# Performance work log

Measured on AMD Instinct MI355X. Metric: run time of the kernel, lower is better.

## Reference

```python
import jax, jax.numpy as jnp
import numpy as np

N = 100000      # nodes
E = 1600000     # edges (avg degree 16)
D_IN = 128
D_H = 128
D_OUT = 64


def setup_inputs() -> dict:
    key = jax.random.key(0)
    ks = jax.random.split(key, 8)
    x = jax.random.normal(ks[0], (N, D_IN), dtype=jnp.float32)
    edge_index = jax.random.randint(ks[1], (2, E), 0, N, dtype=jnp.int64)
    # PyG GraphConv params: lin_rel (with bias) applied to aggregated messages,
    # lin_root (no bias) applied to self features. Kaiming-ish init scale.
    s1 = 1.0 / np.sqrt(D_IN)
    s2 = 1.0 / np.sqrt(D_H)
    W_rel1 = jax.random.uniform(ks[2], (D_H, D_IN), jnp.float32, -s1, s1)
    b_rel1 = jax.random.uniform(ks[3], (D_H,), jnp.float32, -s1, s1)
    W_root1 = jax.random.uniform(ks[4], (D_H, D_IN), jnp.float32, -s1, s1)
    W_rel2 = jax.random.uniform(ks[5], (D_OUT, D_H), jnp.float32, -s2, s2)
    b_rel2 = jax.random.uniform(ks[6], (D_OUT,), jnp.float32, -s2, s2)
    W_root2 = jax.random.uniform(ks[7], (D_OUT, D_H), jnp.float32, -s2, s2)
    return {
        "x": x, "edge_index": edge_index,
        "W_rel1": W_rel1, "b_rel1": b_rel1, "W_root1": W_root1,
        "W_rel2": W_rel2, "b_rel2": b_rel2, "W_root2": W_root2,
    }


def _graph_conv(x, src, dst, W_rel, b_rel, W_root):
    # sum-aggregate neighbor features x[src] into destination nodes,
    # then out = lin_rel(agg) + lin_root(x)  (PyG GraphConv, aggr='add')
    agg = jax.ops.segment_sum(x[src], dst, num_segments=x.shape[0])  # [N, d_in]
    return agg @ W_rel.T + b_rel + x @ W_root.T                      # [N, d_out]


def reference(x, edge_index, W_rel1, b_rel1, W_root1, W_rel2, b_rel2, W_root2):
    src, dst = edge_index[0], edge_index[1]
    h = jax.nn.relu(_graph_conv(x, src, dst, W_rel1, b_rel1, W_root1))  # [N, D_H]
    out = _graph_conv(h, src, dst, W_rel2, b_rel2, W_root2)             # [N, D_OUT]
    # reshape(-1, 1, output_dim) + cat over relations (relations == 1)
    return out.reshape(-1, 1, D_OUT)
```

## Files before the change

### kernel.cpp

```cpp
#include <hip/hip_runtime.h>
#include <hip/hip_bf16.h>


#define BM 128
#define BK 32
#define NPASS 8
#define FILL_GRID 2048

typedef unsigned short ushort_t;

__device__ __forceinline__ ushort_t f2bf(float f) {
    unsigned int u = __float_as_uint(f);
    unsigned int r = (u + 0x7fff + ((u >> 16) & 1)) >> 16;
    return (ushort_t)r;
}

__device__ __forceinline__ float bf2f(ushort_t v) {
    return __uint_as_float(((unsigned int)v) << 16);
}

__device__ __forceinline__ void bf2x(unsigned int v, float& lo, float& hi) {
    lo = __uint_as_float(v << 16);
    hi = __uint_as_float(v & 0xffff0000u);
}


__global__ __launch_bounds__(256) void hist_kernel(const int* __restrict__ dst,
                                                   int* __restrict__ deg, int E, int N) {
    const int pass = blockIdx.x & (NPASS - 1);
    const int chunk = blockIdx.x >> 3;
    const int rangeSize = (N + NPASS - 1) / NPASS;
    const int lo = pass * rangeSize;
    const int hi = (lo + rangeSize < N) ? lo + rangeSize : N;
    const int base = chunk * 1024 + threadIdx.x * 4;
    if (base + 3 < E) {
        const int4 d4 = *(const int4*)(dst + base);
        if (d4.x >= lo && d4.x < hi) atomicAdd(&deg[d4.x], 1);
        if (d4.y >= lo && d4.y < hi) atomicAdd(&deg[d4.y], 1);
        if (d4.z >= lo && d4.z < hi) atomicAdd(&deg[d4.z], 1);
        if (d4.w >= lo && d4.w < hi) atomicAdd(&deg[d4.w], 1);
    } else {
        for (int i = 0; i < 4; ++i) {
            int e = base + i;
            if (e < E) {
                int d = dst[e];
                if (d >= lo && d < hi) atomicAdd(&deg[d], 1);
            }
        }
    }
}

__global__ __launch_bounds__(256) void scan1_kernel(const int* __restrict__ deg,
                                                    int* __restrict__ bsum, int N) {
    int t = threadIdx.x;
    int base = blockIdx.x * 1024 + t * 4;
    int s = 0;
    if (base + 3 < N) {
        int4 v = *(const int4*)(deg + base);
        s = v.x + v.y + v.z + v.w;
    } else {
#pragma unroll
        for (int i = 0; i < 4; ++i)
            if (base + i < N) s += deg[base + i];
    }
#pragma unroll
    for (int d = 32; d > 0; d >>= 1) s += __shfl_down(s, d);
    __shared__ int wsum[4];
    int lane = t & 63, w = t >> 6;
    if (lane == 0) wsum[w] = s;
    __syncthreads();
    if (t == 0) bsum[blockIdx.x] = wsum[0] + wsum[1] + wsum[2] + wsum[3];
}

__global__ __launch_bounds__(256) void scan2_kernel(const int* __restrict__ bsum,
                                                    int* __restrict__ boff,
                                                    int* __restrict__ offN, int B) {
    __shared__ int s[256];
    int t = threadIdx.x;
    int v = (t < B) ? bsum[t] : 0;
    s[t] = v;
    __syncthreads();
    for (int d = 1; d < 256; d <<= 1) {
        int u = (t >= d) ? s[t - d] : 0;
        __syncthreads();
        s[t] += u;
        __syncthreads();
    }
    if (t < B) boff[t] = s[t] - v;
    if (t == B - 1) *offN = s[t];
}

__global__ __launch_bounds__(256) void scan3_kernel(const int* __restrict__ deg,
                                                    const int* __restrict__ boff,
                                                    int* __restrict__ off,
                                                    int* __restrict__ cursor, int N) {
    int t = threadIdx.x;
    int base = blockIdx.x * 1024 + t * 4;
    int d0 = 0, d1 = 0, d2 = 0, d3 = 0;
    if (base + 3 < N) {
        int4 v = *(const int4*)(deg + base);
        d0 = v.x; d1 = v.y; d2 = v.z; d3 = v.w;
    } else {
        if (base + 0 < N) d0 = deg[base + 0];
        if (base + 1 < N) d1 = deg[base + 1];
        if (base + 2 < N) d2 = deg[base + 2];
    }
    int s = d0 + d1 + d2 + d3;
    int lane = t & 63, w = t >> 6;
    int incl = s;
#pragma unroll
    for (int d = 1; d < 64; d <<= 1) {
        int u = __shfl_up(incl, d);
        if (lane >= d) incl += u;
    }
    __shared__ int wsum[4];
    if (lane == 63) wsum[w] = incl;
    __syncthreads();
    int wpre = 0;
#pragma unroll
    for (int i = 0; i < 3; ++i)
        if (i < w) wpre += wsum[i];
    int excl = incl - s + wpre + boff[blockIdx.x];
    int e0 = excl, e1 = e0 + d0, e2 = e1 + d1, e3 = e2 + d2;
    if (base + 3 < N) {
        *(int4*)(off + base) = make_int4(e0, e1, e2, e3);
        *(int4*)(cursor + base) = make_int4(e0, e1, e2, e3);
    } else {
        if (base + 0 < N) { off[base + 0] = e0; cursor[base + 0] = e0; }
        if (base + 1 < N) { off[base + 1] = e1; cursor[base + 1] = e1; }
        if (base + 2 < N) { off[base + 2] = e2; cursor[base + 2] = e2; }
    }
}

__global__ __launch_bounds__(256) void fill_kernel(const int* __restrict__ src,
                                                   const int* __restrict__ dst,
                                                   int* __restrict__ cursor,
                                                   int* __restrict__ csr, int E, int N) {
    const int pass = blockIdx.x & (NPASS - 1);
    const int rangeSize = (N + NPASS - 1) / NPASS;
    const int lo = pass * rangeSize;
    const int hi = (lo + rangeSize < N) ? lo + rangeSize : N;
    const int nChunk = (E + 1023) >> 10;
    for (int chunk = blockIdx.x >> 3; chunk < nChunk; chunk += FILL_GRID / NPASS) {
        const int base = chunk * 1024 + threadIdx.x * 4;
        if (base + 3 < E) {
            const int4 s4 = *(const int4*)(src + base);
            const int4 d4 = *(const int4*)(dst + base);
            if (d4.x >= lo && d4.x < hi) csr[atomicAdd(&cursor[d4.x], 1)] = s4.x;
            if (d4.y >= lo && d4.y < hi) csr[atomicAdd(&cursor[d4.y], 1)] = s4.y;
            if (d4.z >= lo && d4.z < hi) csr[atomicAdd(&cursor[d4.z], 1)] = s4.z;
            if (d4.w >= lo && d4.w < hi) csr[atomicAdd(&cursor[d4.w], 1)] = s4.w;
        } else {
            for (int i = 0; i < 4; ++i) {
                int e = base + i;
                if (e < E) {
                    int d = dst[e];
                    if (d >= lo && d < hi) csr[atomicAdd(&cursor[d], 1)] = src[e];
                }
            }
        }
    }
}


template <int BN, int EPI, int OB, int AB>
__global__ __launch_bounds__(256, 2)
void gemm_k(const float* __restrict__ X, const float* __restrict__ W,
            const void* __restrict__ AGGv, const float* __restrict__ bias,
            void* __restrict__ OUTv, int Nrows) {
    __shared__ float xs[BK][BM + 4];
    __shared__ float wsh[BK][BN + 4];

    const int tid = threadIdx.x;
    const int tc = tid & 15;
    const int tr = tid >> 4;
    const int rowBase = blockIdx.x * BM;
    constexpr int CG = BN / 64;

    float acc[8][4 * CG];
#pragma unroll
    for (int i = 0; i < 8; ++i)
#pragma unroll
        for (int j = 0; j < 4 * CG; ++j) acc[i][j] = 0.f;

    const int srow = tid >> 3;
    const int skq = (tid & 7) * 4;

    for (int kc = 0; kc < 128; kc += BK) {
#pragma unroll
        for (int i = 0; i < 4; ++i) {
            int r = srow + i * 32;
            int g = rowBase + r;
            g = g < Nrows ? g : Nrows - 1;
            const float4 v = *(const float4*)(X + (size_t)g * 128 + kc + skq);
            xs[skq + 0][r] = v.x;
            xs[skq + 1][r] = v.y;
            xs[skq + 2][r] = v.z;
            xs[skq + 3][r] = v.w;
        }
#pragma unroll
        for (int i = 0; i < BN / 32; ++i) {
            int j = srow + i * 32;
            const float4 v = *(const float4*)(W + (size_t)j * 128 + kc + skq);
            wsh[skq + 0][j] = v.x;
            wsh[skq + 1][j] = v.y;
            wsh[skq + 2][j] = v.z;
            wsh[skq + 3][j] = v.w;
        }
        __syncthreads();
#pragma unroll
        for (int k = 0; k < BK; ++k) {
            const float4 xa = *(const float4*)&xs[k][tr * 8];
            const float4 xb = *(const float4*)&xs[k][tr * 8 + 4];
            float xr[8] = {xa.x, xa.y, xa.z, xa.w, xb.x, xb.y, xb.z, xb.w};
            float wv[4 * CG];
            const float4 wa = *(const float4*)&wsh[k][tc * 4];
            wv[0] = wa.x; wv[1] = wa.y; wv[2] = wa.z; wv[3] = wa.w;
            if (CG == 2) {
                const float4 wb = *(const float4*)&wsh[k][64 + tc * 4];
                wv[4] = wb.x; wv[5] = wb.y; wv[6] = wb.z; wv[7] = wb.w;
            }
#pragma unroll
            for (int i = 0; i < 8; ++i)
#pragma unroll
                for (int j = 0; j < 4 * CG; ++j) acc[i][j] += xr[i] * wv[j];
        }
        __syncthreads();
    }

#pragma unroll
    for (int i = 0; i < 8; ++i) {
        int g = rowBase + tr * 8 + i;
        if (g >= Nrows) continue;
#pragma unroll
        for (int cg = 0; cg < CG; ++cg) {
            int c = cg * 64 + tc * 4;
            float4 r;
            r.x = acc[i][cg * 4 + 0];
            r.y = acc[i][cg * 4 + 1];
            r.z = acc[i][cg * 4 + 2];
            r.w = acc[i][cg * 4 + 3];
            if (EPI != 0) {
                float ax, ay, az, aw;
                if (AB) {
                    const ushort_t* A = (const ushort_t*)AGGv;
                    ushort4 a4 = *(const ushort4*)(A + (size_t)g * BN + c);
                    ax = bf2f(a4.x); ay = bf2f(a4.y); az = bf2f(a4.z); aw = bf2f(a4.w);
                } else {
                    const float4 a = *(const float4*)((const float*)AGGv + (size_t)g * BN + c);
                    ax = a.x; ay = a.y; az = a.z; aw = a.w;
                }
                const float4 bb = *(const float4*)(bias + c);
                r.x += ax + bb.x;
                r.y += ay + bb.y;
                r.z += az + bb.z;
                r.w += aw + bb.w;
                if (EPI == 1) {
                    r.x = r.x > 0.f ? r.x : 0.f;
                    r.y = r.y > 0.f ? r.y : 0.f;
                    r.z = r.z > 0.f ? r.z : 0.f;
                    r.w = r.w > 0.f ? r.w : 0.f;
                }
            }
            if (OB) {
                ushort_t* OUT = (ushort_t*)OUTv;
                ushort4 o;
                o.x = f2bf(r.x); o.y = f2bf(r.y); o.z = f2bf(r.z); o.w = f2bf(r.w);
                *(ushort4*)(OUT + (size_t)g * BN + c) = o;
            } else {
                float* OUT = (float*)OUTv;
                *(float4*)(OUT + (size_t)g * BN + c) = r;
            }
        }
    }
}


template <int D, int OB>
__global__ __launch_bounds__(256)
void agg_k(const ushort_t* __restrict__ F, const int* __restrict__ csr,
           const int* __restrict__ off, void* __restrict__ OUTv, int N) {
    constexpr int LPN = (D == 128) ? 32 : 16;
    constexpr int NPB = 256 / LPN;
    int n = blockIdx.x * NPB + (threadIdx.x / LPN);
    if (n >= N) return;
    int lane = threadIdx.x & (LPN - 1);
    int b = off[n], e = off[n + 1];
    const size_t col = (size_t)lane * 4;
    float a0 = 0.f, a1 = 0.f, a2 = 0.f, a3 = 0.f;
    int i = b;
    for (; i + 4 <= e; i += 4) {
        int s0 = csr[i], s1 = csr[i + 1], s2 = csr[i + 2], s3 = csr[i + 3];
        uint2 v0 = *(const uint2*)(F + (size_t)s0 * D + col);
        uint2 v1 = *(const uint2*)(F + (size_t)s1 * D + col);
        uint2 v2 = *(const uint2*)(F + (size_t)s2 * D + col);
        uint2 v3 = *(const uint2*)(F + (size_t)s3 * D + col);
        float l, h;
        bf2x(v0.x, l, h); a0 += l; a1 += h;
        bf2x(v0.y, l, h); a2 += l; a3 += h;
        bf2x(v1.x, l, h); a0 += l; a1 += h;
        bf2x(v1.y, l, h); a2 += l; a3 += h;
        bf2x(v2.x, l, h); a0 += l; a1 += h;
        bf2x(v2.y, l, h); a2 += l; a3 += h;
        bf2x(v3.x, l, h); a0 += l; a1 += h;
        bf2x(v3.y, l, h); a2 += l; a3 += h;
    }
    for (; i < e; ++i) {
        uint2 v = *(const uint2*)(F + (size_t)csr[i] * D + col);
        float l, h;
        bf2x(v.x, l, h); a0 += l; a1 += h;
        bf2x(v.y, l, h); a2 += l; a3 += h;
    }
    if (OB) {
        ushort_t* OUT = (ushort_t*)OUTv;
        ushort4 o;
        o.x = f2bf(a0); o.y = f2bf(a1); o.z = f2bf(a2); o.w = f2bf(a3);
        *(ushort4*)(OUT + (size_t)n * D + col) = o;
    } else {
        float* OUT = (float*)OUTv;
        float4 r; r.x = a0; r.y = a1; r.z = a2; r.w = a3;
        *(float4*)(OUT + (size_t)n * D + col) = r;
    }
}

extern "C" void kernel_launch(void* const* d_in, const int* in_sizes, int n_in,
                              void* d_out, int out_size, void* d_ws, size_t ws_size,
                              hipStream_t stream) {
    const float* x   = (const float*)d_in[0];
    const int*   ei  = (const int*)d_in[1];
    const float* Wr1 = (const float*)d_in[2];
    const float* br1 = (const float*)d_in[3];
    const float* Wo1 = (const float*)d_in[4];
    const float* Wr2 = (const float*)d_in[5];
    const float* br2 = (const float*)d_in[6];
    const float* Wo2 = (const float*)d_in[7];
    float* out = (float*)d_out;

    const int N = in_sizes[0] / 128;
    const int E = in_sizes[1] / 2;

    const int* srcv = ei;
    const int* dstv = ei + E;

    float*    h    = (float*)d_ws;
    ushort_t* qb   = (ushort_t*)(h + (size_t)N * 128);
    ushort_t* a1b  = qb + (size_t)N * 128;
    ushort_t* a2b  = a1b + (size_t)N * 128;
    int*      deg  = (int*)(a2b + (size_t)N * 64);
    int*      off  = deg + N;
    int*      cur  = off + N + 8;
    int*      csr  = cur + N;
    int*      bsum = csr + E;
    int*      boff = bsum + 256;

    const int gemmBlocks = (N + BM - 1) / BM;
    const int agg128Blocks = (N + 7) / 8;
    const int agg64Blocks = (N + 15) / 16;
    const int B = (N + 1023) / 1024;
    const int edgePassBlocks = ((E + 1023) / 1024) * NPASS;

    hipMemsetAsync(deg, 0, (size_t)N * sizeof(int), stream);
    hist_kernel<<<edgePassBlocks, 256, 0, stream>>>(dstv, deg, E, N);
    scan1_kernel<<<B, 256, 0, stream>>>(deg, bsum, N);
    scan2_kernel<<<1, 256, 0, stream>>>(bsum, boff, off + N, B);
    scan3_kernel<<<B, 256, 0, stream>>>(deg, boff, off, cur, N);
    fill_kernel<<<FILL_GRID, 256, 0, stream>>>(srcv, dstv, cur, csr, E, N);

    gemm_k<128, 0, 1, 0><<<gemmBlocks, 256, 0, stream>>>(x, Wr1, nullptr, nullptr, qb, N);
    agg_k<128, 1><<<agg128Blocks, 256, 0, stream>>>(qb, csr, off, a1b, N);
    gemm_k<128, 1, 0, 1><<<gemmBlocks, 256, 0, stream>>>(x, Wo1, a1b, br1, h, N);

    gemm_k<64, 0, 1, 0><<<gemmBlocks, 256, 0, stream>>>(h, Wr2, nullptr, nullptr, qb , N);
    agg_k<64, 1><<<agg64Blocks, 256, 0, stream>>>(qb , csr, off, a2b, N);
    gemm_k<64, 2, 0, 1><<<gemmBlocks, 256, 0, stream>>>(h, Wo2, a2b, br2, out, N);
}
```

Measured before the change: 502.5 us.

## Replace FP32 SIMT GEMMs with concatenated-weight bf16 MFMA GEMMs and separate epilogues

Converts x and weights to bf16 and concatenates the rel and root weight matrices so one MFMA GEMM per layer computes both projections. The bias, aggregation add and ReLU move into standalone elementwise epilogue kernels, and edge-index reads use nontemporal loads. This removes the scalar FP32 FMA GEMM cost and halves GEMM launches, but adds conversion and epilogue passes over memory. The root path now runs in bf16, which lowers precision.

```diff
diff --git a/kernel.cpp b/kernel.cpp
--- a/kernel.cpp
+++ b/kernel.cpp
@@ -2,12 +2,12 @@
 #include <hip/hip_bf16.h>
 
 
-#define BM 128
-#define BK 32
 #define NPASS 8
 #define FILL_GRID 2048
 
 typedef unsigned short ushort_t;
+using bfrag = __attribute__((ext_vector_type(8))) short;
+using f32x4 = __attribute__((ext_vector_type(4))) float;
 
 __device__ __forceinline__ ushort_t f2bf(float f) {
     unsigned int u = __float_as_uint(f);
@@ -22,6 +22,17 @@
 __device__ __forceinline__ void bf2x(unsigned int v, float& lo, float& hi) {
     lo = __uint_as_float(v << 16);
     hi = __uint_as_float(v & 0xffff0000u);
+}
+
+__device__ __forceinline__ int4 ldnt_int4(const int* p) {
+    unsigned long long a = __builtin_nontemporal_load((const unsigned long long*)p);
+    unsigned long long b = __builtin_nontemporal_load(((const unsigned long long*)p) + 1);
+    int4 r;
+    r.x = (int)(unsigned int)(a & 0xffffffffull);
+    r.y = (int)(unsigned int)(a >> 32);
+    r.z = (int)(unsigned int)(b & 0xffffffffull);
+    r.w = (int)(unsigned int)(b >> 32);
+    return r;
 }
 
 
@@ -34,7 +45,7 @@
     const int hi = (lo + rangeSize < N) ? lo + rangeSize : N;
     const int base = chunk * 1024 + threadIdx.x * 4;
     if (base + 3 < E) {
-        const int4 d4 = *(const int4*)(dst + base);
+        const int4 d4 = ldnt_int4(dst + base);
         if (d4.x >= lo && d4.x < hi) atomicAdd(&deg[d4.x], 1);
         if (d4.y >= lo && d4.y < hi) atomicAdd(&deg[d4.y], 1);
         if (d4.z >= lo && d4.z < hi) atomicAdd(&deg[d4.z], 1);
@@ -144,8 +155,8 @@
     for (int chunk = blockIdx.x >> 3; chunk < nChunk; chunk += FILL_GRID / NPASS) {
         const int base = chunk * 1024 + threadIdx.x * 4;
         if (base + 3 < E) {
-            const int4 s4 = *(const int4*)(src + base);
-            const int4 d4 = *(const int4*)(dst + base);
+            const int4 s4 = ldnt_int4(src + base);
+            const int4 d4 = ldnt_int4(dst + base);
             if (d4.x >= lo && d4.x < hi) csr[atomicAdd(&cursor[d4.x], 1)] = s4.x;
             if (d4.y >= lo && d4.y < hi) csr[atomicAdd(&cursor[d4.y], 1)] = s4.y;
             if (d4.z >= lo && d4.z < hi) csr[atomicAdd(&cursor[d4.z], 1)] = s4.z;
@@ -163,113 +174,78 @@
 }
 
 
-template <int BN, int EPI, int OB, int AB>
+__global__ __launch_bounds__(256) void cvt_kernel(const float* __restrict__ in,
+                                                  ushort_t* __restrict__ out, int n) {
+    int base = (blockIdx.x * 256 + threadIdx.x) * 4;
+    if (base + 3 < n) {
+        float4 v = *(const float4*)(in + base);
+        ushort4 o;
+        o.x = f2bf(v.x); o.y = f2bf(v.y); o.z = f2bf(v.z); o.w = f2bf(v.w);
+        *(ushort4*)(out + base) = o;
+    } else {
+        for (int i = 0; i < 4 && base + i < n; ++i) out[base + i] = f2bf(in[base + i]);
+    }
+}
+
+__global__ __launch_bounds__(256) void cvt_w_kernel(const float* __restrict__ Wr1,
+                                                    const float* __restrict__ Wo1,
+                                                    const float* __restrict__ Wr2,
+                                                    const float* __restrict__ Wo2,
+                                                    ushort_t* __restrict__ wcat1,
+                                                    ushort_t* __restrict__ wcat2) {
+    int i = blockIdx.x * 256 + threadIdx.x;
+    if (i < 16384) wcat1[i] = f2bf(Wr1[i]);
+    else if (i < 32768) wcat1[i] = f2bf(Wo1[i - 16384]);
+    else if (i < 40960) wcat2[i - 32768] = f2bf(Wr2[i - 32768]);
+    else if (i < 49152) wcat2[i - 32768] = f2bf(Wo2[i - 40960]);
+}
+
+
+template <int BN, int SPLIT, int O2F>
 __global__ __launch_bounds__(256, 2)
-void gemm_k(const float* __restrict__ X, const float* __restrict__ W,
-            const void* __restrict__ AGGv, const float* __restrict__ bias,
-            void* __restrict__ OUTv, int Nrows) {
-    __shared__ float xs[BK][BM + 4];
-    __shared__ float wsh[BK][BN + 4];
-
-    const int tid = threadIdx.x;
-    const int tc = tid & 15;
-    const int tr = tid >> 4;
-    const int rowBase = blockIdx.x * BM;
-    constexpr int CG = BN / 64;
-
-    float acc[8][4 * CG];
-#pragma unroll
-    for (int i = 0; i < 8; ++i)
-#pragma unroll
-        for (int j = 0; j < 4 * CG; ++j) acc[i][j] = 0.f;
-
-    const int srow = tid >> 3;
-    const int skq = (tid & 7) * 4;
-
-    for (int kc = 0; kc < 128; kc += BK) {
-#pragma unroll
-        for (int i = 0; i < 4; ++i) {
-            int r = srow + i * 32;
-            int g = rowBase + r;
-            g = g < Nrows ? g : Nrows - 1;
-            const float4 v = *(const float4*)(X + (size_t)g * 128 + kc + skq);
-            xs[skq + 0][r] = v.x;
-            xs[skq + 1][r] = v.y;
-            xs[skq + 2][r] = v.z;
-            xs[skq + 3][r] = v.w;
+void mfma_gemm(const ushort_t* __restrict__ A, const ushort_t* __restrict__ Wc,
+               ushort_t* __restrict__ O1, void* __restrict__ O2v, int Nrows) {
+    constexpr int NT = BN / 16;
+    const int w = threadIdx.x >> 6;
+    const int lane = threadIdx.x & 63;
+    const int m0 = blockIdx.x * 64 + w * 16;
+    const int lm = lane & 15;
+    const int lk8 = (lane >> 4) * 8;
+
+    f32x4 acc[NT];
+#pragma unroll
+    for (int t = 0; t < NT; ++t) {
+        acc[t][0] = 0.f; acc[t][1] = 0.f; acc[t][2] = 0.f; acc[t][3] = 0.f;
+    }
+
+    int ar = m0 + lm;
+    ar = ar < Nrows ? ar : Nrows - 1;
+    const ushort_t* Arow = A + (size_t)ar * 128;
+
+#pragma unroll
+    for (int kk = 0; kk < 4; ++kk) {
+        const bfrag af = *(const bfrag*)(Arow + kk * 32 + lk8);
+#pragma unroll
+        for (int t = 0; t < NT; ++t) {
+            const bfrag bf = *(const bfrag*)(Wc + ((size_t)(t * 16 + lm) << 7) + kk * 32 + lk8);
+            acc[t] = __builtin_amdgcn_mfma_f32_16x16x32_bf16(af, bf, acc[t], 0, 0, 0);
         }
-#pragma unroll
-        for (int i = 0; i < BN / 32; ++i) {
-            int j = srow + i * 32;
-            const float4 v = *(const float4*)(W + (size_t)j * 128 + kc + skq);
-            wsh[skq + 0][j] = v.x;
-            wsh[skq + 1][j] = v.y;
-            wsh[skq + 2][j] = v.z;
-            wsh[skq + 3][j] = v.w;
-        }
-        __syncthreads();
-#pragma unroll
-        for (int k = 0; k < BK; ++k) {
-            const float4 xa = *(const float4*)&xs[k][tr * 8];
-            const float4 xb = *(const float4*)&xs[k][tr * 8 + 4];
-            float xr[8] = {xa.x, xa.y, xa.z, xa.w, xb.x, xb.y, xb.z, xb.w};
-            float wv[4 * CG];
-            const float4 wa = *(const float4*)&wsh[k][tc * 4];
-            wv[0] = wa.x; wv[1] = wa.y; wv[2] = wa.z; wv[3] = wa.w;
-            if (CG == 2) {
-                const float4 wb = *(const float4*)&wsh[k][64 + tc * 4];
-                wv[4] = wb.x; wv[5] = wb.y; wv[6] = wb.z; wv[7] = wb.w;
-            }
-#pragma unroll
-            for (int i = 0; i < 8; ++i)
-#pragma unroll
-                for (int j = 0; j < 4 * CG; ++j) acc[i][j] += xr[i] * wv[j];
-        }
-        __syncthreads();
-    }
-
-#pragma unroll
-    for (int i = 0; i < 8; ++i) {
-        int g = rowBase + tr * 8 + i;
-        if (g >= Nrows) continue;
-#pragma unroll
-        for (int cg = 0; cg < CG; ++cg) {
-            int c = cg * 64 + tc * 4;
-            float4 r;
-            r.x = acc[i][cg * 4 + 0];
-            r.y = acc[i][cg * 4 + 1];
-            r.z = acc[i][cg * 4 + 2];
-            r.w = acc[i][cg * 4 + 3];
-            if (EPI != 0) {
-                float ax, ay, az, aw;
-                if (AB) {
-                    const ushort_t* A = (const ushort_t*)AGGv;
-                    ushort4 a4 = *(const ushort4*)(A + (size_t)g * BN + c);
-                    ax = bf2f(a4.x); ay = bf2f(a4.y); az = bf2f(a4.z); aw = bf2f(a4.w);
-                } else {
-                    const float4 a = *(const float4*)((const float*)AGGv + (size_t)g * BN + c);
-                    ax = a.x; ay = a.y; az = a.z; aw = a.w;
-                }
-                const float4 bb = *(const float4*)(bias + c);
-                r.x += ax + bb.x;
-                r.y += ay + bb.y;
-                r.z += az + bb.z;
-                r.w += aw + bb.w;
-                if (EPI == 1) {
-                    r.x = r.x > 0.f ? r.x : 0.f;
-                    r.y = r.y > 0.f ? r.y : 0.f;
-                    r.z = r.z > 0.f ? r.z : 0.f;
-                    r.w = r.w > 0.f ? r.w : 0.f;
-                }
-            }
-            if (OB) {
-                ushort_t* OUT = (ushort_t*)OUTv;
-                ushort4 o;
-                o.x = f2bf(r.x); o.y = f2bf(r.y); o.z = f2bf(r.z); o.w = f2bf(r.w);
-                *(ushort4*)(OUT + (size_t)g * BN + c) = o;
+    }
+
+    const int rbase = m0 + (lane >> 4) * 4;
+#pragma unroll
+    for (int t = 0; t < NT; ++t) {
+        const int col = t * 16 + lm;
+#pragma unroll
+        for (int r = 0; r < 4; ++r) {
+            const int row = rbase + r;
+            if (row >= Nrows) continue;
+            const float v = acc[t][r];
+            if (col < SPLIT) {
+                O1[(size_t)row * SPLIT + col] = f2bf(v);
             } else {
-                float* OUT = (float*)OUTv;
-                *(float4*)(OUT + (size_t)g * BN + c) = r;
+                if (O2F) ((float*)O2v)[(size_t)row * (BN - SPLIT) + (col - SPLIT)] = v;
+                else ((ushort_t*)O2v)[(size_t)row * (BN - SPLIT) + (col - SPLIT)] = f2bf(v);
             }
         }
     }
@@ -323,6 +299,69 @@
     }
 }
 
+
+__global__ __launch_bounds__(256) void epi1_kernel(const ushort_t* __restrict__ a1,
+                                                   const ushort_t* __restrict__ hpre,
+                                                   const float* __restrict__ b1,
+                                                   ushort_t* __restrict__ h, int total) {
+    int base = (blockIdx.x * 256 + threadIdx.x) * 8;
+    if (base + 7 >= total) {
+        for (int i = 0; i < 8 && base + i < total; ++i) {
+            float v = bf2f(a1[base + i]) + b1[(base + i) & 127] + bf2f(hpre[base + i]);
+            h[base + i] = f2bf(v > 0.f ? v : 0.f);
+        }
+        return;
+    }
+    uint4 av = *(const uint4*)(a1 + base);
+    uint4 pv = *(const uint4*)(hpre + base);
+    int c0 = base & 127;
+    float4 bA = *(const float4*)(b1 + c0);
+    float4 bB = *(const float4*)(b1 + c0 + 4);
+    float bb[8] = {bA.x, bA.y, bA.z, bA.w, bB.x, bB.y, bB.z, bB.w};
+    unsigned int aw[4] = {av.x, av.y, av.z, av.w};
+    unsigned int pw[4] = {pv.x, pv.y, pv.z, pv.w};
+    ushort4 o[2];
+    ushort_t res[8];
+#pragma unroll
+    for (int q = 0; q < 4; ++q) {
+        float al, ah, pl, ph;
+        bf2x(aw[q], al, ah);
+        bf2x(pw[q], pl, ph);
+        float v0 = al + bb[q * 2 + 0] + pl;
+        float v1 = ah + bb[q * 2 + 1] + ph;
+        res[q * 2 + 0] = f2bf(v0 > 0.f ? v0 : 0.f);
+        res[q * 2 + 1] = f2bf(v1 > 0.f ? v1 : 0.f);
+    }
+    o[0].x = res[0]; o[0].y = res[1]; o[0].z = res[2]; o[0].w = res[3];
+    o[1].x = res[4]; o[1].y = res[5]; o[1].z = res[6]; o[1].w = res[7];
+    *(ushort4*)(h + base) = o[0];
+    *(ushort4*)(h + base + 4) = o[1];
+}
+
+__global__ __launch_bounds__(256) void epi2_kernel(const ushort_t* __restrict__ a2,
+                                                   const float* __restrict__ opre,
+                                                   const float* __restrict__ b2,
+                                                   float* __restrict__ out, int total) {
+    int base = (blockIdx.x * 256 + threadIdx.x) * 4;
+    if (base + 3 >= total) {
+        for (int i = 0; i < 4 && base + i < total; ++i)
+            out[base + i] = bf2f(a2[base + i]) + b2[(base + i) & 63] + opre[base + i];
+        return;
+    }
+    uint2 av = *(const uint2*)(a2 + base);
+    float4 ov = *(const float4*)(opre + base);
+    float4 bv = *(const float4*)(b2 + (base & 63));
+    float al, ah, bl, bh;
+    bf2x(av.x, al, ah);
+    bf2x(av.y, bl, bh);
+    float4 r;
+    r.x = al + bv.x + ov.x;
+    r.y = ah + bv.y + ov.y;
+    r.z = bl + bv.z + ov.z;
+    r.w = bh + bv.w + ov.w;
+    *(float4*)(out + base) = r;
+}
+
 extern "C" void kernel_launch(void* const* d_in, const int* in_sizes, int n_in,
                               void* d_out, int out_size, void* d_ws, size_t ws_size,
                               hipStream_t stream) {
@@ -342,22 +381,27 @@
     const int* srcv = ei;
     const int* dstv = ei + E;
 
-    float*    h    = (float*)d_ws;
-    ushort_t* qb   = (ushort_t*)(h + (size_t)N * 128);
-    ushort_t* a1b  = qb + (size_t)N * 128;
-    ushort_t* a2b  = a1b + (size_t)N * 128;
-    int*      deg  = (int*)(a2b + (size_t)N * 64);
+    ushort_t* bufA = (ushort_t*)d_ws;
+    ushort_t* bufB = bufA + (size_t)N * 128;
+    ushort_t* bufC = bufB + (size_t)N * 128;
+    ushort_t* bufD = bufC + (size_t)N * 128;
+    ushort_t* wcat1 = bufD + (size_t)N * 128;
+    ushort_t* wcat2 = wcat1 + 256 * 128;
+    int*      deg  = (int*)(wcat2 + 128 * 128);
     int*      off  = deg + N;
     int*      cur  = off + N + 8;
     int*      csr  = cur + N;
     int*      bsum = csr + E;
     int*      boff = bsum + 256;
 
-    const int gemmBlocks = (N + BM - 1) / BM;
+    const int B = (N + 1023) / 1024;
+    const int edgePassBlocks = ((E + 1023) / 1024) * NPASS;
+    const int gemmBlocks = (N + 63) / 64;
     const int agg128Blocks = (N + 7) / 8;
     const int agg64Blocks = (N + 15) / 16;
-    const int B = (N + 1023) / 1024;
-    const int edgePassBlocks = ((E + 1023) / 1024) * NPASS;
+    const int cvtXBlocks = (N * 128 / 4 + 255) / 256;
+    const int epi1Blocks = (N * 128 / 8 + 255) / 256;
+    const int epi2Blocks = (N * 64 / 4 + 255) / 256;
 
     hipMemsetAsync(deg, 0, (size_t)N * sizeof(int), stream);
     hist_kernel<<<edgePassBlocks, 256, 0, stream>>>(dstv, deg, E, N);
@@ -366,11 +410,16 @@
     scan3_kernel<<<B, 256, 0, stream>>>(deg, boff, off, cur, N);
     fill_kernel<<<FILL_GRID, 256, 0, stream>>>(srcv, dstv, cur, csr, E, N);
 
-    gemm_k<128, 0, 1, 0><<<gemmBlocks, 256, 0, stream>>>(x, Wr1, nullptr, nullptr, qb, N);
-    agg_k<128, 1><<<agg128Blocks, 256, 0, stream>>>(qb, csr, off, a1b, N);
-    gemm_k<128, 1, 0, 1><<<gemmBlocks, 256, 0, stream>>>(x, Wo1, a1b, br1, h, N);
-
-    gemm_k<64, 0, 1, 0><<<gemmBlocks, 256, 0, stream>>>(h, Wr2, nullptr, nullptr, qb , N);
-    agg_k<64, 1><<<agg64Blocks, 256, 0, stream>>>(qb , csr, off, a2b, N);
-    gemm_k<64, 2, 0, 1><<<gemmBlocks, 256, 0, stream>>>(h, Wo2, a2b, br2, out, N);
-}
+    cvt_kernel<<<cvtXBlocks, 256, 0, stream>>>(x, bufA , N * 128);
+    cvt_w_kernel<<<192, 256, 0, stream>>>(Wr1, Wo1, Wr2, Wo2, wcat1, wcat2);
+
+    mfma_gemm<256, 128, 0><<<gemmBlocks, 256, 0, stream>>>(bufA, wcat1, bufB ,
+                                                           bufC , N);
+    agg_k<128, 1><<<agg128Blocks, 256, 0, stream>>>(bufB, csr, off, bufD , N);
+    epi1_kernel<<<epi1Blocks, 256, 0, stream>>>(bufD, bufC, br1, bufA , N * 128);
+
+    mfma_gemm<128, 64, 1><<<gemmBlocks, 256, 0, stream>>>(bufA, wcat2, bufB ,
+                                                          bufC , N);
+    agg_k<64, 1><<<agg64Blocks, 256, 0, stream>>>(bufB, csr, off, bufD , N);
+    epi2_kernel<<<epi2Blocks, 256, 0, stream>>>(bufD, (const float*)bufC, br2, out, N * 64);
+}
```

After: 473.2 us. -5.8%, faster.
